# Performance work log

Hardware: AMD Instinct MI355X
Metric: run time of the kernel (lower is better)

The kernel has to match this reference:

```python
import jax, jax.numpy as jnp
import numpy as np

G, NPG = 100, 500
N = G * NPG            # 50000 nodes, contiguous equal-size graphs
IN, H = 128, 256
L = 3                  # num_layers
K = 3                  # knn k (loop=True -> self included)
E = 16 * N             # 800000 edges

def setup_inputs():
    key = jax.random.key(0)
    k = jax.random.split(key, 8)
    x = jax.random.normal(k[0], (N, IN), jnp.float32)
    batch = jnp.repeat(jnp.arange(G, dtype=jnp.int32), NPG)
    gid = jax.random.randint(k[1], (E,), 0, G)
    src = jax.random.randint(k[2], (E,), 0, NPG) + gid * NPG
    dst = jax.random.randint(k[3], (E,), 0, NPG) + gid * NPG
    edge_index = jnp.stack([src, dst]).astype(jnp.int32)
    def lin(kk, fin, fout):
        return (jax.random.normal(kk, (fin, fout), jnp.float32) / np.sqrt(fin)).astype(jnp.float32)
    inp = dict(x=x, edge_index=edge_index, batch=batch)
    inp["emb_W"] = lin(k[4], IN, H); inp["emb_b"] = jnp.zeros((H,), jnp.float32)
    inp["conv_W"] = jnp.stack([lin(jax.random.fold_in(k[5], i), H, H) for i in range(L)])
    inp["conv_b"] = jnp.zeros((L, H), jnp.float32)
    inp["fconv_W"] = jnp.stack([lin(jax.random.fold_in(k[6], i), H, H) for i in range(L)])
    inp["fconv_b"] = jnp.zeros((L, H), jnp.float32)
    inp["norm_w"] = jnp.ones((L, H), jnp.float32); inp["norm_b"] = jnp.zeros((L, H), jnp.float32); inp["norm_ms"] = jnp.ones((L, H), jnp.float32)
    inp["fnorm_w"] = jnp.ones((L, H), jnp.float32); inp["fnorm_b"] = jnp.zeros((L, H), jnp.float32); inp["fnorm_ms"] = jnp.ones((L, H), jnp.float32)
    inp["gate_W"] = lin(k[7], 2 * H, H); inp["gate_b"] = jnp.zeros((H,), jnp.float32)
    return inp

def _gcn_conv(h, src, dst, W, b):
    # GCNConv: add self loops, symmetric deg^-1/2 normalization
    m = h @ W                                     # [N,H]
    loop = jnp.arange(N, dtype=src.dtype)
    s2 = jnp.concatenate([src, loop]); d2 = jnp.concatenate([dst, loop])
    deg = jax.ops.segment_sum(jnp.ones_like(d2, jnp.float32), d2, num_segments=N)
    dinv = jnp.where(deg > 0, jax.lax.rsqrt(deg), 0.0)
    coef = (dinv[s2] * dinv[d2])[:, None]
    return jax.ops.segment_sum(m[s2] * coef, d2, num_segments=N) + b

def _graph_norm(x, batch, w, b, ms, cnt):
    # PyG GraphNorm: out = w * (x - ms*mean) / sqrt(var + eps) + b, per-graph stats
    mean = jax.ops.segment_sum(x, batch, num_segments=G) / cnt
    out = x - mean[batch] * ms
    var = jax.ops.segment_sum(out * out, batch, num_segments=G) / cnt
    return w * out * jax.lax.rsqrt(var + 1e-5)[batch] + b

def _knn_graph(x):
    # per-graph cosine knn, loop=True (self has sim 1 and is kept)
    xr = x.reshape(G, NPG, -1)
    xn = xr / (jnp.linalg.norm(xr, axis=-1, keepdims=True) + 1e-12)
    sim = jnp.einsum('gnh,gmh->gnm', xn, xn)      # [G,NPG,NPG]
    _, idx = jax.lax.top_k(sim, K)                # [G,NPG,K]
    offs = (jnp.arange(G) * NPG)[:, None, None]
    src = (idx + offs).reshape(-1)
    dst = jnp.broadcast_to(jnp.arange(N).reshape(G, NPG, 1), (G, NPG, K)).reshape(-1)
    return src.astype(jnp.int32), dst.astype(jnp.int32)

def reference(x, edge_index, batch, emb_W, emb_b, conv_W, conv_b, norm_w, norm_b, norm_ms, fconv_W, fconv_b, fnorm_w, fnorm_b, fnorm_ms, gate_W, gate_b):
    cnt = jax.ops.segment_sum(jnp.ones((N,), jnp.float32), batch, num_segments=G)[:, None]
    h = x @ emb_W + emb_b
    fsrc, fdst = _knn_graph(h)
    src, dst = edge_index[0], edge_index[1]
    all_x = []
    for i in range(L - 1):   # eval mode: dropout is identity
        prev = h
        h = _gcn_conv(h, src, dst, conv_W[i], conv_b[i])
        h = jax.nn.leaky_relu(_graph_norm(h, batch, norm_w[i], norm_b[i], norm_ms[i], cnt))
        f = _gcn_conv(h, fsrc, fdst, fconv_W[i], fconv_b[i])
        f = jax.nn.leaky_relu(_graph_norm(f, batch, fnorm_w[i], fnorm_b[i], fnorm_ms[i], cnt))
        gate = jax.nn.sigmoid(jnp.concatenate([h, f], axis=-1) @ gate_W + gate_b)
        h = gate * h + (1.0 - gate) * f + prev
        all_x.append(h)
    # faithful to source: for i in range(L): += pool(all_x[i-1])  (Python negative indexing!)
    gf = jnp.zeros((G, H), jnp.float32)
    for i in range(L):
        gf = gf + jax.ops.segment_sum(all_x[i - 1], batch, num_segments=G) / cnt
    return gf
```

## Files before the change

### kernel.cpp

```cpp
#include <hip/hip_runtime.h>
#include <math.h>

#define NN 50000
#define GG 100
#define NPGc 500
#define HH 256
#define IND 128

typedef __attribute__((ext_vector_type(8))) short short8v;
typedef __attribute__((ext_vector_type(4))) float f32x4;

__device__ __forceinline__ ushort f2bf(float f) {
    union { float f; unsigned u; } v; v.f = f;
    unsigned r = (v.u + 0x7fffu + ((v.u >> 16) & 1u)) >> 16;
    return (ushort)r;
}
__device__ __forceinline__ float bf2f(ushort h) {
    union { unsigned u; float f; } v; v.u = ((unsigned)h) << 16;
    return v.f;
}

__device__ __forceinline__ int swz(int row, int kidx) { return kidx ^ ((row & 7) << 3); }

__global__ void wcvt(const float* __restrict__ src, ushort* __restrict__ dst, int K, int N)
{
    int i = blockIdx.x * 256 + threadIdx.x;
    if (i < K * N) {
        int n = i / K, k = i % K;
        dst[i] = f2bf(src[(size_t)k * N + n]);
    }
}

__global__ __launch_bounds__(256)
void gemm_mfma(const float* __restrict__ A, const float* __restrict__ A2,
               const ushort* __restrict__ Wt, const float* __restrict__ bias,
               float* __restrict__ C, int M, int K, int lda, int mode,
               const float* __restrict__ hn, const float* __restrict__ fn,
               const float* __restrict__ prev)
{
    __shared__ ushort As[128][64];
    __shared__ ushort Bs[128][64];
    const int tid = threadIdx.x;
    const int lane = tid & 63;
    const int w = tid >> 6;
    const int wr = (w >> 1) * 64, wc = (w & 1) * 64;
    const int row0 = blockIdx.x * 128, col0 = blockIdx.y * 128;
    const int lr = lane & 15, lk = (lane >> 4) * 8;
    f32x4 acc[4][4] = {};

    for (int k0 = 0; k0 < K; k0 += 64) {
        __syncthreads();
        #pragma unroll
        for (int it = 0; it < 4; ++it) {
            int c = it * 256 + tid;
            int row = c >> 3, col = (c & 7) * 8;
            int gr = row0 + row; if (gr > M - 1) gr = M - 1;
            const float* Ap = A; int kk = k0 + col;
            if (A2 != nullptr && kk >= 256) { Ap = A2; kk -= 256; }
            const float* s = &Ap[(size_t)gr * lda + kk];
            float4 v0 = *(const float4*)s;
            float4 v1 = *(const float4*)(s + 4);
            union { ushort u[8]; int4 q; } pk;
            pk.u[0] = f2bf(v0.x); pk.u[1] = f2bf(v0.y); pk.u[2] = f2bf(v0.z); pk.u[3] = f2bf(v0.w);
            pk.u[4] = f2bf(v1.x); pk.u[5] = f2bf(v1.y); pk.u[6] = f2bf(v1.z); pk.u[7] = f2bf(v1.w);
            *(int4*)&As[row][swz(row, col)] = pk.q;
        }
        #pragma unroll
        for (int it = 0; it < 4; ++it) {
            int c = it * 256 + tid;
            int n = c >> 3, k = (c & 7) * 8;
            *(int4*)&Bs[n][swz(n, k)] = *(const int4*)&Wt[(size_t)(col0 + n) * K + k0 + k];
        }
        __syncthreads();
        #pragma unroll
        for (int ks = 0; ks < 2; ++ks) {
            short8v av[4], bv[4];
            #pragma unroll
            for (int m = 0; m < 4; ++m) {
                int rr = wr + m * 16 + lr;
                av[m] = *(const short8v*)&As[rr][swz(rr, ks * 32 + lk)];
            }
            #pragma unroll
            for (int n = 0; n < 4; ++n) {
                int rr = wc + n * 16 + lr;
                bv[n] = *(const short8v*)&Bs[rr][swz(rr, ks * 32 + lk)];
            }
            #pragma unroll
            for (int m = 0; m < 4; ++m)
                #pragma unroll
                for (int n = 0; n < 4; ++n)
                    acc[m][n] = __builtin_amdgcn_mfma_f32_16x16x32_bf16(av[m], bv[n], acc[m][n], 0, 0, 0);
        }
    }
    const int fr = (lane >> 4) * 4;
    if (mode == 0) {
        #pragma unroll
        for (int n = 0; n < 4; ++n) {
            int col = col0 + wc + n * 16 + lr;
            float bb = bias ? bias[col] : 0.f;
            #pragma unroll
            for (int m = 0; m < 4; ++m) {
                int rbase = row0 + wr + m * 16 + fr;
                #pragma unroll
                for (int r = 0; r < 4; ++r) {
                    int row = rbase + r;
                    if (row < M) C[(size_t)row * HH + col] = acc[m][n][r] + bb;
                }
            }
        }
    } else {
        #pragma unroll
        for (int n = 0; n < 4; ++n) {
            int col = col0 + wc + n * 16 + lr;
            float gb = bias[col];
            #pragma unroll
            for (int m = 0; m < 4; ++m) {
                int rbase = row0 + wr + m * 16 + fr;
                #pragma unroll
                for (int r = 0; r < 4; ++r) {
                    int row = rbase + r;
                    if (row < M) {
                        size_t o = (size_t)row * HH + col;
                        float z = acc[m][n][r] + gb;
                        float s = 1.f / (1.f + expf(-z));
                        C[o] = s * hn[o] + (1.f - s) * fn[o] + prev[o];
                    }
                }
            }
        }
    }
}

__global__ __launch_bounds__(256)
void row_norm_hl(const float* __restrict__ h, ushort* __restrict__ xh, ushort* __restrict__ xl)
{
    int n = blockIdx.x, c = threadIdx.x;
    float v = h[(size_t)n * HH + c];
    __shared__ float red[256];
    red[c] = v * v;
    __syncthreads();
    for (int s = 128; s > 0; s >>= 1) {
        if (c < s) red[c] += red[c + s];
        __syncthreads();
    }
    float norm = sqrtf(red[0]);
    float xn = v / (norm + 1e-12f);
    ushort hi = f2bf(xn);
    xh[(size_t)n * HH + c] = hi;
    xl[(size_t)n * HH + c] = f2bf(xn - bf2f(hi));
}

__device__ __forceinline__ bool tk_better(float va, int ia, float vb, int ib)
{
    return (va > vb) || (va == vb && ia < ib);
}

__device__ __forceinline__ void ins3(float v, int i,
                                     float& a0, int& b0, float& a1, int& b1,
                                     float& a2, int& b2)
{
    if (tk_better(v, i, a0, b0))      { a2 = a1; b2 = b1; a1 = a0; b1 = b0; a0 = v; b0 = i; }
    else if (tk_better(v, i, a1, b1)) { a2 = a1; b2 = b1; a1 = v;  b1 = i; }
    else if (tk_better(v, i, a2, b2)) { a2 = v;  b2 = i; }
}

__device__ __forceinline__ void merge3(float& v0, float& v1, float& v2,
                                       int& i0, int& i1, int& i2, int off)
{
    float w0 = __shfl_xor(v0, off), w1 = __shfl_xor(v1, off), w2 = __shfl_xor(v2, off);
    int   j0 = __shfl_xor(i0, off), j1 = __shfl_xor(i1, off), j2 = __shfl_xor(i2, off);
    float avv[3] = { v0, v1, v2 }, bvv[3] = { w0, w1, w2 };
    int   aii[3] = { i0, i1, i2 }, bii[3] = { j0, j1, j2 };
    float rv[3]; int ri[3];
    int p = 0, q = 0;
    #pragma unroll
    for (int t = 0; t < 3; ++t) {
        bool takeA = tk_better(avv[p], aii[p], bvv[q], bii[q]);
        rv[t] = takeA ? avv[p] : bvv[q];
        ri[t] = takeA ? aii[p] : bii[q];
        if (takeA) ++p; else ++q;
    }
    v0 = rv[0]; v1 = rv[1]; v2 = rv[2];
    i0 = ri[0]; i1 = ri[1]; i2 = ri[2];
}

__global__ __launch_bounds__(256, 2)
void simtopk(const ushort* __restrict__ xnh, const ushort* __restrict__ xnl,
             int* __restrict__ fsrc)
{
    __shared__ ushort Ash[128][64], Asl[128][64], Bsh[128][64], Bsl[128][64];
    const int g = blockIdx.y;
    const int row0 = blockIdx.x * 128;
    const int tid = threadIdx.x;
    const int lane = tid & 63;
    const int w = tid >> 6;
    const int wrow = w * 32;
    const int lr = lane & 15;
    const int hi4 = lane >> 4;
    const int lk = hi4 * 8;
    const size_t base = (size_t)g * NPGc * HH;

    float tv0[2][4], tv1[2][4], tv2[2][4];
    int   ti0[2][4], ti1[2][4], ti2[2][4];
    #pragma unroll
    for (int m = 0; m < 2; ++m)
        #pragma unroll
        for (int r = 0; r < 4; ++r) {
            tv0[m][r] = tv1[m][r] = tv2[m][r] = -2.f;
            ti0[m][r] = ti1[m][r] = ti2[m][r] = 0x7fffffff;
        }

    for (int ct = 0; ct < 4; ++ct) {
        const int col0 = ct * 128;
        f32x4 acc[2][8] = {};
        for (int k0 = 0; k0 < HH; k0 += 64) {
            __syncthreads();
            #pragma unroll
            for (int it = 0; it < 4; ++it) {
                int c = it * 256 + tid;
                int rr = c >> 3, kc = (c & 7) * 8;
                int grow = row0 + rr; if (grow > NPGc - 1) grow = NPGc - 1;
                const size_t o = base + (size_t)grow * HH + k0 + kc;
                *(int4*)&Ash[rr][swz(rr, kc)] = *(const int4*)(xnh + o);
                *(int4*)&Asl[rr][swz(rr, kc)] = *(const int4*)(xnl + o);
            }
            #pragma unroll
            for (int it = 0; it < 4; ++it) {
                int c = it * 256 + tid;
                int rr = c >> 3, kc = (c & 7) * 8;
                int gcol = col0 + rr; if (gcol > NPGc - 1) gcol = NPGc - 1;
                const size_t o = base + (size_t)gcol * HH + k0 + kc;
                *(int4*)&Bsh[rr][swz(rr, kc)] = *(const int4*)(xnh + o);
                *(int4*)&Bsl[rr][swz(rr, kc)] = *(const int4*)(xnl + o);
            }
            __syncthreads();
            #pragma unroll
            for (int ks = 0; ks < 2; ++ks) {
                short8v ah[2], al[2], bh[8], bl[8];
                #pragma unroll
                for (int m = 0; m < 2; ++m) {
                    int rr = wrow + m * 16 + lr;
                    ah[m] = *(const short8v*)&Ash[rr][swz(rr, ks * 32 + lk)];
                    al[m] = *(const short8v*)&Asl[rr][swz(rr, ks * 32 + lk)];
                }
                #pragma unroll
                for (int n = 0; n < 8; ++n) {
                    int rr = n * 16 + lr;
                    bh[n] = *(const short8v*)&Bsh[rr][swz(rr, ks * 32 + lk)];
                    bl[n] = *(const short8v*)&Bsl[rr][swz(rr, ks * 32 + lk)];
                }
                #pragma unroll
                for (int m = 0; m < 2; ++m)
                    #pragma unroll
                    for (int n = 0; n < 8; ++n) {
                        acc[m][n] = __builtin_amdgcn_mfma_f32_16x16x32_bf16(ah[m], bh[n], acc[m][n], 0, 0, 0);
                        acc[m][n] = __builtin_amdgcn_mfma_f32_16x16x32_bf16(ah[m], bl[n], acc[m][n], 0, 0, 0);
                        acc[m][n] = __builtin_amdgcn_mfma_f32_16x16x32_bf16(al[m], bh[n], acc[m][n], 0, 0, 0);
                    }
            }
        }
        #pragma unroll
        for (int m = 0; m < 2; ++m)
            #pragma unroll
            for (int n = 0; n < 8; ++n) {
                int col = col0 + n * 16 + lr;
                if (col < NPGc) {
                    #pragma unroll
                    for (int r = 0; r < 4; ++r)
                        ins3(acc[m][n][r], col,
                             tv0[m][r], ti0[m][r], tv1[m][r], ti1[m][r], tv2[m][r], ti2[m][r]);
                }
            }
    }

    #pragma unroll
    for (int m = 0; m < 2; ++m)
        #pragma unroll
        for (int r = 0; r < 4; ++r) {
            #pragma unroll
            for (int off = 1; off <= 8; off <<= 1)
                merge3(tv0[m][r], tv1[m][r], tv2[m][r],
                       ti0[m][r], ti1[m][r], ti2[m][r], off);
        }

    if (lr == 0) {
        #pragma unroll
        for (int m = 0; m < 2; ++m)
            #pragma unroll
            for (int r = 0; r < 4; ++r) {
                int row = row0 + wrow + m * 16 + hi4 * 4 + r;
                if (row < NPGc) {
                    int rg = g * NPGc + row;
                    fsrc[rg * 3 + 0] = g * NPGc + ti0[m][r];
                    fsrc[rg * 3 + 1] = g * NPGc + ti1[m][r];
                    fsrc[rg * 3 + 2] = g * NPGc + ti2[m][r];
                }
            }
    }
}

__global__ void hist_kernel(const int* __restrict__ dst, int* __restrict__ cnt, int nE)
{
    int e = blockIdx.x * 256 + threadIdx.x;
    if (e < nE) atomicAdd(&cnt[dst[e]], 1);
}

__global__ void scan1_kernel(const int* __restrict__ in, int* __restrict__ out,
                             int* __restrict__ bsum, int n)
{
    __shared__ int sh[256];
    int t = threadIdx.x;
    int i = blockIdx.x * 256 + t;
    int v = (i < n) ? in[i] : 0;
    sh[t] = v;
    __syncthreads();
    for (int s = 1; s < 256; s <<= 1) {
        int tv = (t >= s) ? sh[t - s] : 0;
        __syncthreads();
        sh[t] += tv;
        __syncthreads();
    }
    if (i < n) out[i] = sh[t] - v;
    if (t == 255) bsum[blockIdx.x] = sh[255];
}

__global__ void scan2_kernel(int* __restrict__ bsum, int nb)
{
    __shared__ int sh[256];
    int t = threadIdx.x;
    int v = (t < nb) ? bsum[t] : 0;
    sh[t] = v;
    __syncthreads();
    for (int s = 1; s < 256; s <<= 1) {
        int tv = (t >= s) ? sh[t - s] : 0;
        __syncthreads();
        sh[t] += tv;
        __syncthreads();
    }
    if (t < nb) bsum[t] = sh[t] - v;
}

__global__ void scan3_kernel(int* __restrict__ out, const int* __restrict__ bsum, int n)
{
    int i = blockIdx.x * 256 + threadIdx.x;
    if (i < n) out[i] += bsum[blockIdx.x];
}

__global__ void fill_kernel(const int* __restrict__ src, const int* __restrict__ dst,
                            const int* __restrict__ row_ptr, int* __restrict__ cursor,
                            int* __restrict__ sorted_src, int nE)
{
    int e = blockIdx.x * 256 + threadIdx.x;
    if (e < nE) {
        int d = dst[e];
        int pos = row_ptr[d] + atomicAdd(&cursor[d], 1);
        sorted_src[pos] = src[e];
    }
}

__global__ void dinv_kernel(const int* __restrict__ cnt, float* __restrict__ dinv, int n)
{
    int i = blockIdx.x * 256 + threadIdx.x;
    if (i < n) dinv[i] = rsqrtf((float)cnt[i] + 1.0f);
}

__global__ __launch_bounds__(256)
void gcn_gather(const float* __restrict__ m, const int* __restrict__ row_ptr,
                const int* __restrict__ cnt, const int* __restrict__ srcs,
                const float* __restrict__ dinv, const float* __restrict__ bias,
                float* __restrict__ out)
{
    int n = blockIdx.x, c = threadIdx.x;
    float dn = dinv[n];
    float acc = m[(size_t)n * HH + c] * dn;
    int s0 = row_ptr[n], e0 = s0 + cnt[n];
    for (int e = s0; e < e0; ++e) {
        int s = srcs[e];
        acc += m[(size_t)s * HH + c] * dinv[s];
    }
    out[(size_t)n * HH + c] = acc * dn + bias[c];
}

__global__ __launch_bounds__(256)
void fgcn_gather(const float* __restrict__ m, const int* __restrict__ fsrc,
                 const float* __restrict__ bias, float* __restrict__ out)
{
    int n = blockIdx.x, c = threadIdx.x;
    int s0 = fsrc[n * 3], s1 = fsrc[n * 3 + 1], s2 = fsrc[n * 3 + 2];
    float acc = m[(size_t)n * HH + c] + m[(size_t)s0 * HH + c]
              + m[(size_t)s1 * HH + c] + m[(size_t)s2 * HH + c];
    out[(size_t)n * HH + c] = 0.25f * acc + bias[c];
}

__global__ __launch_bounds__(256)
void norm_stats(const float* __restrict__ x, float* __restrict__ S1, float* __restrict__ S2)
{
    int g = blockIdx.x, chunk = blockIdx.y, c = threadIdx.x;
    int r0 = chunk * 63, r1 = min(r0 + 63, NPGc);
    float s1 = 0.f, s2 = 0.f;
    for (int r = r0; r < r1; ++r) {
        float v = x[((size_t)(g * NPGc + r)) * HH + c];
        s1 += v; s2 += v * v;
    }
    atomicAdd(&S1[g * HH + c], s1);
    atomicAdd(&S2[g * HH + c], s2);
}

__global__ __launch_bounds__(256)
void norm_apply(float* __restrict__ x, const float* __restrict__ S1, const float* __restrict__ S2,
                const float* __restrict__ w, const float* __restrict__ b,
                const float* __restrict__ ms)
{
    int n = blockIdx.x, c = threadIdx.x;
    int g = n / NPGc;
    size_t o = (size_t)n * HH + c;
    float v = x[o];
    float mean = S1[g * HH + c] / (float)NPGc;
    float mm = mean * ms[c];
    float var = S2[g * HH + c] / (float)NPGc - 2.f * mm * mean + mm * mm;
    float outv = w[c] * (v - mm) * rsqrtf(var + 1e-5f) + b[c];
    x[o] = outv > 0.f ? outv : 0.01f * outv;
}

__global__ __launch_bounds__(256)
void pool_kernel(const float* __restrict__ X0, const float* __restrict__ X1,
                 float* __restrict__ out)
{
    int g = blockIdx.x, c = threadIdx.x;
    float s0 = 0.f, s1 = 0.f;
    for (int r = 0; r < NPGc; ++r) {
        size_t o = ((size_t)(g * NPGc + r)) * HH + c;
        s0 += X0[o];
        s1 += X1[o];
    }
    out[g * HH + c] = (s0 + 2.f * s1) / (float)NPGc;
}

__global__ void sentinel_kernel(float* out, int n)
{
    int i = blockIdx.x * 256 + threadIdx.x;
    if (i < n) out[i] = 12345.0f;
}

extern "C" void kernel_launch(void* const* d_in, const int* in_sizes, int n_in,
                              void* d_out, int out_size, void* d_ws, size_t ws_size,
                              hipStream_t stream)
{
    const float* x       = (const float*)d_in[0];
    const int* edge_idx  = (const int*)d_in[1];
    const float* emb_W   = (const float*)d_in[3];
    const float* emb_b   = (const float*)d_in[4];
    const float* conv_W  = (const float*)d_in[5];
    const float* conv_b  = (const float*)d_in[6];
    const float* fconv_W = (const float*)d_in[7];
    const float* fconv_b = (const float*)d_in[8];
    const float* norm_w  = (const float*)d_in[9];
    const float* norm_b  = (const float*)d_in[10];
    const float* norm_ms = (const float*)d_in[11];
    const float* fnorm_w = (const float*)d_in[12];
    const float* fnorm_b = (const float*)d_in[13];
    const float* fnorm_ms= (const float*)d_in[14];
    const float* gate_W  = (const float*)d_in[15];
    const float* gate_b  = (const float*)d_in[16];

    const int E = in_sizes[1] / 2;
    const int* esrc = edge_idx;
    const int* edst = edge_idx + E;

    const size_t NHf = (size_t)NN * HH;
    char* p = (char*)d_ws;
    auto alloc = [&](size_t bytes) { char* r = p; p += (bytes + 255) & ~(size_t)255; return r; };
    float* B0 = (float*)alloc(NHf * 4);
    float* B1 = (float*)alloc(NHf * 4);
    float* B2 = (float*)alloc(NHf * 4);
    float* B3 = (float*)alloc(NHf * 4);
    ushort* xnh = (ushort*)B2;
    ushort* xnl = xnh + NHf;
    int* sorted_src = (int*)alloc((size_t)E * 4);
    int* row_ptr    = (int*)alloc((size_t)NN * 4);
    int* deg_cnt    = (int*)alloc((size_t)NN * 4);
    int* cursor     = (int*)alloc((size_t)NN * 4);
    float* dinv     = (float*)alloc((size_t)NN * 4);
    int* fsrc       = (int*)alloc((size_t)NN * 3 * 4);
    float* S1       = (float*)alloc((size_t)GG * HH * 4);
    float* S2       = (float*)alloc((size_t)GG * HH * 4);
    int* bsum       = (int*)alloc(1024);
    ushort* wts     = (ushort*)alloc((size_t)425984 * 2);
    size_t needed = (size_t)(p - (char*)d_ws);
    if (ws_size < needed) {
        sentinel_kernel<<<(out_size + 255) / 256, 256, 0, stream>>>((float*)d_out, out_size);
        return;
    }
    ushort* embWt   = wts;
    ushort* convWt0 = wts + 32768;
    ushort* convWt1 = wts + 32768 + 65536;
    ushort* fconvWt0 = wts + 163840;
    ushort* fconvWt1 = wts + 163840 + 65536;
    ushort* gateWt  = wts + 294912;

    const int nScanB = (NN + 255) / 256;

    hipMemsetAsync(deg_cnt, 0, (size_t)NN * 4, stream);
    hipMemsetAsync(cursor, 0, (size_t)NN * 4, stream);

    wcvt<<<(32768 + 255) / 256, 256, 0, stream>>>(emb_W, embWt, IND, HH);
    wcvt<<<(65536 + 255) / 256, 256, 0, stream>>>(conv_W, convWt0, HH, HH);
    wcvt<<<(65536 + 255) / 256, 256, 0, stream>>>(conv_W + 65536, convWt1, HH, HH);
    wcvt<<<(65536 + 255) / 256, 256, 0, stream>>>(fconv_W, fconvWt0, HH, HH);
    wcvt<<<(65536 + 255) / 256, 256, 0, stream>>>(fconv_W + 65536, fconvWt1, HH, HH);
    wcvt<<<(131072 + 255) / 256, 256, 0, stream>>>(gate_W, gateWt, 2 * HH, HH);

    dim3 ggrid((NN + 127) / 128, 2);
    gemm_mfma<<<ggrid, 256, 0, stream>>>(x, nullptr, embWt, emb_b, B0, NN, IND, IND, 0,
                                         nullptr, nullptr, nullptr);

    hist_kernel<<<(E + 255) / 256, 256, 0, stream>>>(edst, deg_cnt, E);
    scan1_kernel<<<nScanB, 256, 0, stream>>>(deg_cnt, row_ptr, bsum, NN);
    scan2_kernel<<<1, 256, 0, stream>>>(bsum, nScanB);
    scan3_kernel<<<nScanB, 256, 0, stream>>>(row_ptr, bsum, NN);
    fill_kernel<<<(E + 255) / 256, 256, 0, stream>>>(esrc, edst, row_ptr, cursor, sorted_src, E);
    dinv_kernel<<<(NN + 255) / 256, 256, 0, stream>>>(deg_cnt, dinv, NN);

    row_norm_hl<<<NN, 256, 0, stream>>>(B0, xnh, xnl);
    dim3 sgrid(4, GG);
    simtopk<<<sgrid, 256, 0, stream>>>(xnh, xnl, fsrc);

    float* h  = B0;
    float* mb = B1;
    dim3 ngrid(GG, 8);
    for (int i = 0; i < 2; ++i) {
        const ushort* Wc = (i == 0) ? convWt0 : convWt1;
        const ushort* Wf = (i == 0) ? fconvWt0 : fconvWt1;
        const float* bc  = conv_b  + (size_t)i * HH;
        const float* bf  = fconv_b + (size_t)i * HH;
        gemm_mfma<<<ggrid, 256, 0, stream>>>(h, nullptr, Wc, nullptr, mb, NN, HH, HH, 0,
                                             nullptr, nullptr, nullptr);
        gcn_gather<<<NN, 256, 0, stream>>>(mb, row_ptr, deg_cnt, sorted_src, dinv, bc, B2);
        hipMemsetAsync(S1, 0, (size_t)2 * GG * HH * 4, stream);
        norm_stats<<<ngrid, 256, 0, stream>>>(B2, S1, S2);
        norm_apply<<<NN, 256, 0, stream>>>(B2, S1, S2, norm_w + i * HH, norm_b + i * HH,
                                           norm_ms + i * HH);
        gemm_mfma<<<ggrid, 256, 0, stream>>>(B2, nullptr, Wf, nullptr, mb, NN, HH, HH, 0,
                                             nullptr, nullptr, nullptr);
        fgcn_gather<<<NN, 256, 0, stream>>>(mb, fsrc, bf, B3);
        hipMemsetAsync(S1, 0, (size_t)2 * GG * HH * 4, stream);
        norm_stats<<<ngrid, 256, 0, stream>>>(B3, S1, S2);
        norm_apply<<<NN, 256, 0, stream>>>(B3, S1, S2, fnorm_w + i * HH, fnorm_b + i * HH,
                                           fnorm_ms + i * HH);
        gemm_mfma<<<ggrid, 256, 0, stream>>>(B2, B3, gateWt, gate_b, mb, NN, 2 * HH, HH, 1,
                                             B2, B3, h);
        float* t = h; h = mb; mb = t;
    }
    pool_kernel<<<GG, 256, 0, stream>>>(mb, h, (float*)d_out);
}
```

Baseline: 1.392 ms.

## Split kNN top-k across column tiles and fuse GCN gathers with norm statistics

```diff
diff --git a/kernel.cpp b/kernel.cpp
--- a/kernel.cpp
+++ b/kernel.cpp
@@ -185,12 +185,18 @@
 }
 
 __global__ __launch_bounds__(256, 2)
-void simtopk(const ushort* __restrict__ xnh, const ushort* __restrict__ xnl,
-             int* __restrict__ fsrc)
+void simtopk_tile(const ushort* __restrict__ xnh, const ushort* __restrict__ xnl,
+                  float* __restrict__ cval, int* __restrict__ cidx)
 {
     __shared__ ushort Ash[128][64], Asl[128][64], Bsh[128][64], Bsl[128][64];
-    const int g = blockIdx.y;
-    const int row0 = blockIdx.x * 128;
+    const int flat = blockIdx.x;
+    const int xcd = flat & 7, rest = flat >> 3;
+    const int t = rest & 15;
+    const int g = (rest >> 4) * 8 + xcd;
+    if (g >= GG) return;
+    const int row0 = (t & 3) * 128;
+    const int cx = t >> 2;
+    const int col0 = cx * 128;
     const int tid = threadIdx.x;
     const int lane = tid & 63;
     const int w = tid >> 6;
@@ -210,68 +216,65 @@
             ti0[m][r] = ti1[m][r] = ti2[m][r] = 0x7fffffff;
         }
 
-    for (int ct = 0; ct < 4; ++ct) {
-        const int col0 = ct * 128;
-        f32x4 acc[2][8] = {};
-        for (int k0 = 0; k0 < HH; k0 += 64) {
-            __syncthreads();
-            #pragma unroll
-            for (int it = 0; it < 4; ++it) {
-                int c = it * 256 + tid;
-                int rr = c >> 3, kc = (c & 7) * 8;
-                int grow = row0 + rr; if (grow > NPGc - 1) grow = NPGc - 1;
-                const size_t o = base + (size_t)grow * HH + k0 + kc;
-                *(int4*)&Ash[rr][swz(rr, kc)] = *(const int4*)(xnh + o);
-                *(int4*)&Asl[rr][swz(rr, kc)] = *(const int4*)(xnl + o);
-            }
-            #pragma unroll
-            for (int it = 0; it < 4; ++it) {
-                int c = it * 256 + tid;
-                int rr = c >> 3, kc = (c & 7) * 8;
-                int gcol = col0 + rr; if (gcol > NPGc - 1) gcol = NPGc - 1;
-                const size_t o = base + (size_t)gcol * HH + k0 + kc;
-                *(int4*)&Bsh[rr][swz(rr, kc)] = *(const int4*)(xnh + o);
-                *(int4*)&Bsl[rr][swz(rr, kc)] = *(const int4*)(xnl + o);
-            }
-            __syncthreads();
-            #pragma unroll
-            for (int ks = 0; ks < 2; ++ks) {
-                short8v ah[2], al[2], bh[8], bl[8];
-                #pragma unroll
-                for (int m = 0; m < 2; ++m) {
-                    int rr = wrow + m * 16 + lr;
-                    ah[m] = *(const short8v*)&Ash[rr][swz(rr, ks * 32 + lk)];
-                    al[m] = *(const short8v*)&Asl[rr][swz(rr, ks * 32 + lk)];
-                }
+    f32x4 acc[2][8] = {};
+    for (int k0 = 0; k0 < HH; k0 += 64) {
+        __syncthreads();
+        #pragma unroll
+        for (int it = 0; it < 4; ++it) {
+            int c = it * 256 + tid;
+            int rr = c >> 3, kc = (c & 7) * 8;
+            int grow = row0 + rr; if (grow > NPGc - 1) grow = NPGc - 1;
+            const size_t o = base + (size_t)grow * HH + k0 + kc;
+            *(int4*)&Ash[rr][swz(rr, kc)] = *(const int4*)(xnh + o);
+            *(int4*)&Asl[rr][swz(rr, kc)] = *(const int4*)(xnl + o);
+        }
+        #pragma unroll
+        for (int it = 0; it < 4; ++it) {
+            int c = it * 256 + tid;
+            int rr = c >> 3, kc = (c & 7) * 8;
+            int gcol = col0 + rr; if (gcol > NPGc - 1) gcol = NPGc - 1;
+            const size_t o = base + (size_t)gcol * HH + k0 + kc;
+            *(int4*)&Bsh[rr][swz(rr, kc)] = *(const int4*)(xnh + o);
+            *(int4*)&Bsl[rr][swz(rr, kc)] = *(const int4*)(xnl + o);
+        }
+        __syncthreads();
+        #pragma unroll
+        for (int ks = 0; ks < 2; ++ks) {
+            short8v ah[2], al[2], bh[8], bl[8];
+            #pragma unroll
+            for (int m = 0; m < 2; ++m) {
+                int rr = wrow + m * 16 + lr;
+                ah[m] = *(const short8v*)&Ash[rr][swz(rr, ks * 32 + lk)];
+                al[m] = *(const short8v*)&Asl[rr][swz(rr, ks * 32 + lk)];
+            }
+            #pragma unroll
+            for (int n = 0; n < 8; ++n) {
+                int rr = n * 16 + lr;
+                bh[n] = *(const short8v*)&Bsh[rr][swz(rr, ks * 32 + lk)];
+                bl[n] = *(const short8v*)&Bsl[rr][swz(rr, ks * 32 + lk)];
+            }
+            #pragma unroll
+            for (int m = 0; m < 2; ++m)
                 #pragma unroll
                 for (int n = 0; n < 8; ++n) {
-                    int rr = n * 16 + lr;
-                    bh[n] = *(const short8v*)&Bsh[rr][swz(rr, ks * 32 + lk)];
-                    bl[n] = *(const short8v*)&Bsl[rr][swz(rr, ks * 32 + lk)];
+                    acc[m][n] = __builtin_amdgcn_mfma_f32_16x16x32_bf16(ah[m], bh[n], acc[m][n], 0, 0, 0);
+                    acc[m][n] = __builtin_amdgcn_mfma_f32_16x16x32_bf16(ah[m], bl[n], acc[m][n], 0, 0, 0);
+                    acc[m][n] = __builtin_amdgcn_mfma_f32_16x16x32_bf16(al[m], bh[n], acc[m][n], 0, 0, 0);
                 }
+        }
+    }
+    #pragma unroll
+    for (int m = 0; m < 2; ++m)
+        #pragma unroll
+        for (int n = 0; n < 8; ++n) {
+            int col = col0 + n * 16 + lr;
+            if (col < NPGc) {
                 #pragma unroll
-                for (int m = 0; m < 2; ++m)
-                    #pragma unroll
-                    for (int n = 0; n < 8; ++n) {
-                        acc[m][n] = __builtin_amdgcn_mfma_f32_16x16x32_bf16(ah[m], bh[n], acc[m][n], 0, 0, 0);
-                        acc[m][n] = __builtin_amdgcn_mfma_f32_16x16x32_bf16(ah[m], bl[n], acc[m][n], 0, 0, 0);
-                        acc[m][n] = __builtin_amdgcn_mfma_f32_16x16x32_bf16(al[m], bh[n], acc[m][n], 0, 0, 0);
-                    }
-            }
-        }
-        #pragma unroll
-        for (int m = 0; m < 2; ++m)
-            #pragma unroll
-            for (int n = 0; n < 8; ++n) {
-                int col = col0 + n * 16 + lr;
-                if (col < NPGc) {
-                    #pragma unroll
-                    for (int r = 0; r < 4; ++r)
-                        ins3(acc[m][n][r], col,
-                             tv0[m][r], ti0[m][r], tv1[m][r], ti1[m][r], tv2[m][r], ti2[m][r]);
-                }
-            }
-    }
+                for (int r = 0; r < 4; ++r)
+                    ins3(acc[m][n][r], col,
+                         tv0[m][r], ti0[m][r], tv1[m][r], ti1[m][r], tv2[m][r], ti2[m][r]);
+            }
+        }
 
     #pragma unroll
     for (int m = 0; m < 2; ++m)
@@ -290,13 +293,32 @@
             for (int r = 0; r < 4; ++r) {
                 int row = row0 + wrow + m * 16 + hi4 * 4 + r;
                 if (row < NPGc) {
-                    int rg = g * NPGc + row;
-                    fsrc[rg * 3 + 0] = g * NPGc + ti0[m][r];
-                    fsrc[rg * 3 + 1] = g * NPGc + ti1[m][r];
-                    fsrc[rg * 3 + 2] = g * NPGc + ti2[m][r];
+                    size_t o = ((size_t)(g * NPGc + row)) * 12 + cx * 3;
+                    cval[o + 0] = tv0[m][r]; cidx[o + 0] = ti0[m][r];
+                    cval[o + 1] = tv1[m][r]; cidx[o + 1] = ti1[m][r];
+                    cval[o + 2] = tv2[m][r]; cidx[o + 2] = ti2[m][r];
                 }
             }
     }
+}
+
+__global__ void cand_merge(const float* __restrict__ cval, const int* __restrict__ cidx,
+                           int* __restrict__ fsrc)
+{
+    int row = blockIdx.x * 256 + threadIdx.x;
+    if (row >= NN) return;
+    int g = row / NPGc;
+    float v0 = -3.f, v1 = -3.f, v2 = -3.f;
+    int i0 = 0x7fffffff, i1 = 0x7fffffff, i2 = 0x7fffffff;
+    #pragma unroll
+    for (int j = 0; j < 12; ++j) {
+        float v = cval[(size_t)row * 12 + j];
+        int   i = cidx[(size_t)row * 12 + j];
+        ins3(v, i, v0, i0, v1, i1, v2, i2);
+    }
+    fsrc[row * 3 + 0] = g * NPGc + i0;
+    fsrc[row * 3 + 1] = g * NPGc + i1;
+    fsrc[row * 3 + 2] = g * NPGc + i2;
 }
 
 __global__ void hist_kernel(const int* __restrict__ dst, int* __restrict__ cnt, int nE)
@@ -365,45 +387,121 @@
 }
 
 __global__ __launch_bounds__(256)
-void gcn_gather(const float* __restrict__ m, const int* __restrict__ row_ptr,
-                const int* __restrict__ cnt, const int* __restrict__ srcs,
-                const float* __restrict__ dinv, const float* __restrict__ bias,
-                float* __restrict__ out)
-{
-    int n = blockIdx.x, c = threadIdx.x;
-    float dn = dinv[n];
-    float acc = m[(size_t)n * HH + c] * dn;
-    int s0 = row_ptr[n], e0 = s0 + cnt[n];
-    for (int e = s0; e < e0; ++e) {
-        int s = srcs[e];
-        acc += m[(size_t)s * HH + c] * dinv[s];
-    }
-    out[(size_t)n * HH + c] = acc * dn + bias[c];
+void gcn32(const float* __restrict__ m, const int* __restrict__ row_ptr,
+           const int* __restrict__ cnt, const int* __restrict__ srcs,
+           const float* __restrict__ dinv, const float* __restrict__ bias,
+           float* __restrict__ out, float* __restrict__ S1, float* __restrict__ S2)
+{
+    __shared__ float ml[NPGc][32];
+    __shared__ float dl[NPGc];
+    __shared__ int   idxb[4][2][32];
+    __shared__ float s1sh[4][32], s2sh[4][32];
+    const int cc = blockIdx.x, g = blockIdx.y;
+    const int tid = threadIdx.x, lane = tid & 63, w = tid >> 6;
+    const int c2 = lane & 31, p = lane >> 5;
+    const int nbase = g * NPGc;
+    const int ch0 = cc * 32;
+
+    #pragma unroll
+    for (int i = 0; i < 16; ++i) {
+        int flat = i * 256 + tid;
+        if (flat < NPGc * 8) {
+            int row = flat >> 3, q = flat & 7;
+            *(float4*)&ml[row][q * 4] =
+                *(const float4*)&m[((size_t)(nbase + row)) * HH + ch0 + q * 4];
+        }
+    }
+    for (int i = tid; i < NPGc; i += 256) dl[i] = dinv[nbase + i];
+    __syncthreads();
+
+    const float bb = bias[ch0 + c2];
+    float s1 = 0.f, s2 = 0.f;
+    const int n0w = w * 125, n1w = n0w + 125;
+    for (int n0 = n0w; n0 < n1w; n0 += 2) {
+        int myn = n0 + p;
+        bool valid = myn < n1w;
+        int nn = valid ? myn : n0;
+        int s0 = row_ptr[nbase + nn];
+        int dg = valid ? cnt[nbase + nn] : 0;
+        float dn = dl[nn];
+        float acc = ml[nn][c2] * dn;
+        for (int bse = 0; bse < dg; bse += 32) {
+            int chunk = dg - bse; if (chunk > 32) chunk = 32;
+            if (c2 < chunk) idxb[w][p][c2] = srcs[s0 + bse + c2] - nbase;
+            for (int e = 0; e < chunk; ++e) {
+                int sl = idxb[w][p][e];
+                acc += ml[sl][c2] * dl[sl];
+            }
+        }
+        float outv = acc * dn + bb;
+        if (valid) {
+            out[((size_t)(nbase + nn)) * HH + ch0 + c2] = outv;
+            s1 += outv; s2 += outv * outv;
+        }
+    }
+    s1 += __shfl_xor(s1, 32);
+    s2 += __shfl_xor(s2, 32);
+    if (p == 0) { s1sh[w][c2] = s1; s2sh[w][c2] = s2; }
+    __syncthreads();
+    if (tid < 32) {
+        float a = s1sh[0][tid] + s1sh[1][tid] + s1sh[2][tid] + s1sh[3][tid];
+        float b = s2sh[0][tid] + s2sh[1][tid] + s2sh[2][tid] + s2sh[3][tid];
+        S1[g * HH + ch0 + tid] = a;
+        S2[g * HH + ch0 + tid] = b;
+    }
 }
 
 __global__ __launch_bounds__(256)
-void fgcn_gather(const float* __restrict__ m, const int* __restrict__ fsrc,
-                 const float* __restrict__ bias, float* __restrict__ out)
-{
-    int n = blockIdx.x, c = threadIdx.x;
-    int s0 = fsrc[n * 3], s1 = fsrc[n * 3 + 1], s2 = fsrc[n * 3 + 2];
-    float acc = m[(size_t)n * HH + c] + m[(size_t)s0 * HH + c]
-              + m[(size_t)s1 * HH + c] + m[(size_t)s2 * HH + c];
-    out[(size_t)n * HH + c] = 0.25f * acc + bias[c];
-}
-
-__global__ __launch_bounds__(256)
-void norm_stats(const float* __restrict__ x, float* __restrict__ S1, float* __restrict__ S2)
-{
-    int g = blockIdx.x, chunk = blockIdx.y, c = threadIdx.x;
-    int r0 = chunk * 63, r1 = min(r0 + 63, NPGc);
+void fgcn32(const float* __restrict__ m, const int* __restrict__ fsrc,
+            const float* __restrict__ bias, float* __restrict__ out,
+            float* __restrict__ S1, float* __restrict__ S2)
+{
+    __shared__ float ml[NPGc][32];
+    __shared__ float s1sh[4][32], s2sh[4][32];
+    const int cc = blockIdx.x, g = blockIdx.y;
+    const int tid = threadIdx.x, lane = tid & 63, w = tid >> 6;
+    const int c2 = lane & 31, p = lane >> 5;
+    const int nbase = g * NPGc;
+    const int ch0 = cc * 32;
+
+    #pragma unroll
+    for (int i = 0; i < 16; ++i) {
+        int flat = i * 256 + tid;
+        if (flat < NPGc * 8) {
+            int row = flat >> 3, q = flat & 7;
+            *(float4*)&ml[row][q * 4] =
+                *(const float4*)&m[((size_t)(nbase + row)) * HH + ch0 + q * 4];
+        }
+    }
+    __syncthreads();
+
+    const float bb = bias[ch0 + c2];
     float s1 = 0.f, s2 = 0.f;
-    for (int r = r0; r < r1; ++r) {
-        float v = x[((size_t)(g * NPGc + r)) * HH + c];
-        s1 += v; s2 += v * v;
-    }
-    atomicAdd(&S1[g * HH + c], s1);
-    atomicAdd(&S2[g * HH + c], s2);
+    const int n0w = w * 125, n1w = n0w + 125;
+    for (int n0 = n0w; n0 < n1w; n0 += 2) {
+        int myn = n0 + p;
+        bool valid = myn < n1w;
+        int nn = valid ? myn : n0;
+        int b3 = (nbase + nn) * 3;
+        int a0 = fsrc[b3 + 0] - nbase;
+        int a1 = fsrc[b3 + 1] - nbase;
+        int a2 = fsrc[b3 + 2] - nbase;
+        float outv = 0.25f * (ml[nn][c2] + ml[a0][c2] + ml[a1][c2] + ml[a2][c2]) + bb;
+        if (valid) {
+            out[((size_t)(nbase + nn)) * HH + ch0 + c2] = outv;
+            s1 += outv; s2 += outv * outv;
+        }
+    }
+    s1 += __shfl_xor(s1, 32);
+    s2 += __shfl_xor(s2, 32);
+    if (p == 0) { s1sh[w][c2] = s1; s2sh[w][c2] = s2; }
+    __syncthreads();
+    if (tid < 32) {
+        float a = s1sh[0][tid] + s1sh[1][tid] + s1sh[2][tid] + s1sh[3][tid];
+        float b = s2sh[0][tid] + s2sh[1][tid] + s2sh[2][tid] + s2sh[3][tid];
+        S1[g * HH + ch0 + tid] = a;
+        S2[g * HH + ch0 + tid] = b;
+    }
 }
 
 __global__ __launch_bounds__(256)
@@ -486,6 +584,8 @@
     float* S2       = (float*)alloc((size_t)GG * HH * 4);
     int* bsum       = (int*)alloc(1024);
     ushort* wts     = (ushort*)alloc((size_t)425984 * 2);
+    float* cval     = (float*)alloc((size_t)NN * 12 * 4);
+    int*   cidx     = (int*)alloc((size_t)NN * 12 * 4);
     size_t needed = (size_t)(p - (char*)d_ws);
     if (ws_size < needed) {
         sentinel_kernel<<<(out_size + 255) / 256, 256, 0, stream>>>((float*)d_out, out_size);
@@ -522,12 +622,12 @@
     dinv_kernel<<<(NN + 255) / 256, 256, 0, stream>>>(deg_cnt, dinv, NN);
 
     row_norm_hl<<<NN, 256, 0, stream>>>(B0, xnh, xnl);
-    dim3 sgrid(4, GG);
-    simtopk<<<sgrid, 256, 0, stream>>>(xnh, xnl, fsrc);
+    simtopk_tile<<<1664, 256, 0, stream>>>(xnh, xnl, cval, cidx);
+    cand_merge<<<(NN + 255) / 256, 256, 0, stream>>>(cval, cidx, fsrc);
 
     float* h  = B0;
     float* mb = B1;
-    dim3 ngrid(GG, 8);
+    dim3 sgrid8(8, GG);
     for (int i = 0; i < 2; ++i) {
         const ushort* Wc = (i == 0) ? convWt0 : convWt1;
         const ushort* Wf = (i == 0) ? fconvWt0 : fconvWt1;
@@ -535,16 +635,13 @@
         const float* bf  = fconv_b + (size_t)i * HH;
         gemm_mfma<<<ggrid, 256, 0, stream>>>(h, nullptr, Wc, nullptr, mb, NN, HH, HH, 0,
                                              nullptr, nullptr, nullptr);
-        gcn_gather<<<NN, 256, 0, stream>>>(mb, row_ptr, deg_cnt, sorted_src, dinv, bc, B2);
-        hipMemsetAsync(S1, 0, (size_t)2 * GG * HH * 4, stream);
-        norm_stats<<<ngrid, 256, 0, stream>>>(B2, S1, S2);
+        gcn32<<<sgrid8, 256, 0, stream>>>(mb, row_ptr, deg_cnt, sorted_src, dinv, bc,
+                                          B2, S1, S2);
         norm_apply<<<NN, 256, 0, stream>>>(B2, S1, S2, norm_w + i * HH, norm_b + i * HH,
                                            norm_ms + i * HH);
         gemm_mfma<<<ggrid, 256, 0, stream>>>(B2, nullptr, Wf, nullptr, mb, NN, HH, HH, 0,
                                              nullptr, nullptr, nullptr);
-        fgcn_gather<<<NN, 256, 0, stream>>>(mb, fsrc, bf, B3);
-        hipMemsetAsync(S1, 0, (size_t)2 * GG * HH * 4, stream);
-        norm_stats<<<ngrid, 256, 0, stream>>>(B3, S1, S2);
+        fgcn32<<<sgrid8, 256, 0, stream>>>(mb, fsrc, bf, B3, S1, S2);
         norm_apply<<<NN, 256, 0, stream>>>(B3, S1, S2, fnorm_w + i * HH, fnorm_b + i * HH,
                                            fnorm_ms + i * HH);
         gemm_mfma<<<ggrid, 256, 0, stream>>>(B2, B3, gateWt, gate_b, mb, NN, 2 * HH, HH, 1,
```

Result: slower. 1.669 ms (+19.8%).
